# Kernel tuning notes

Measured on AMD Instinct MI355X. Metric: run time of the kernel, lower is better.

## Reference

```python
import jax, jax.numpy as jnp
import numpy as np

HIDDEN_DIM = 4096
NUM_EXPERTS = 64
TOP_K = 8
ROUTED_SCALING_FACTOR = 2.5
NUM_TOKENS = 16384


def setup_inputs() -> dict:
    key = jax.random.key(0)
    kx, kw = jax.random.split(key)
    x = jax.random.normal(kx, (NUM_TOKENS, HIDDEN_DIM), dtype=jnp.float32)
    # gate Linear weight (no bias): torch Linear stores [out, in]; we keep [in, out] for x @ W
    W = jax.random.normal(kw, (HIDDEN_DIM, NUM_EXPERTS), dtype=jnp.float32) * (1.0 / np.sqrt(HIDDEN_DIM))
    e_score_correction_bias = jnp.zeros((NUM_EXPERTS,), dtype=jnp.float32)
    return {"x": x, "W": W, "e_score_correction_bias": e_score_correction_bias}


def reference(x, W, e_score_correction_bias):
    # logits: [T, E]
    logits = jnp.einsum("td,de->te", x, W)
    scores = jax.nn.sigmoid(logits)
    scores_with_bias = scores + e_score_correction_bias
    # top-k over experts (sorted descending, matches torch.topk sorted=True)
    _, topk_indices = jax.lax.top_k(scores_with_bias, TOP_K)  # [T, k]
    # gather the UNBIASED scores at the selected experts
    topk_scores = jnp.take_along_axis(scores, topk_indices, axis=-1)  # [T, k]
    scores_sum = jnp.sum(topk_scores, axis=-1, keepdims=True) + 1e-20
    topk_weights = topk_scores / scores_sum * ROUTED_SCALING_FACTOR
    return topk_indices, topk_weights
```

## Files before the change

### kernel.cpp

```cpp
#include <hip/hip_runtime.h>
#include <math.h>

#define NT 16384
#define HD 4096
#define NE 64
#define TT 32
#define DC 64
#define NCH (HD / DC)
#define SXS 34
#define SLS 65
#define GAP_THRESH 4e-5f

__device__ __forceinline__ float fsig(float z) { return 1.0f / (1.0f + expf(-z)); }
__device__ __forceinline__ double dsig(double z) { return 1.0 / (1.0 + exp(-z)); }

__global__ __launch_bounds__(256) void moe_gate_f32(
    const float* __restrict__ X, const float* __restrict__ Wg,
    const float* __restrict__ bias, float* __restrict__ out,
    unsigned int* __restrict__ nflag, int* __restrict__ flags) {
  __shared__ float sX[DC][SXS];
  __shared__ float sW[DC][NE];
  __shared__ float sL[TT][SLS];
  __shared__ float sB[NE];

  const int tid   = threadIdx.x;
  const int tok0  = blockIdx.x * TT;
  const int tr    = tid >> 4;
  const int tc    = tid & 15;
  const int tok_s = tid >> 3;
  const int dv    = tid & 7;

  if (tid < NE) sB[tid] = bias[tid];

  float acc[2][4];
#pragma unroll
  for (int i = 0; i < 2; ++i)
#pragma unroll
    for (int j = 0; j < 4; ++j) acc[i][j] = 0.0f;

  const float* xrow = X + (size_t)(tok0 + tok_s) * HD + dv * 8;

  float4 xr[2], wr[4];
#pragma unroll
  for (int s = 0; s < 2; ++s) xr[s] = *(const float4*)(xrow + s * 4);
#pragma unroll
  for (int s = 0; s < 4; ++s)
    wr[s] = *(const float4*)(Wg + (size_t)(tid + 256 * s) * 4);

  for (int k = 0; k < NCH; ++k) {
    __syncthreads();
#pragma unroll
    for (int s = 0; s < 2; ++s) {
      const int d = dv * 8 + s * 4;
      sX[d + 0][tok_s] = xr[s].x;
      sX[d + 1][tok_s] = xr[s].y;
      sX[d + 2][tok_s] = xr[s].z;
      sX[d + 3][tok_s] = xr[s].w;
    }
#pragma unroll
    for (int s = 0; s < 4; ++s) {
      const int f = (tid + 256 * s) * 4;
      *(float4*)&sW[f >> 6][f & 63] = wr[s];
    }
    __syncthreads();
    if (k + 1 < NCH) {
      const float* xp = xrow + (k + 1) * DC;
      const float* wp = Wg + (size_t)(k + 1) * (DC * NE);
#pragma unroll
      for (int s = 0; s < 2; ++s) xr[s] = *(const float4*)(xp + s * 4);
#pragma unroll
      for (int s = 0; s < 4; ++s)
        wr[s] = *(const float4*)(wp + (size_t)(tid + 256 * s) * 4);
    }
#pragma unroll
    for (int dd = 0; dd < DC; ++dd) {
      const float2 xa = *(const float2*)&sX[dd][tr * 2];
      const float4 wa = *(const float4*)&sW[dd][tc * 4];
      acc[0][0] += xa.x * wa.x; acc[0][1] += xa.x * wa.y;
      acc[0][2] += xa.x * wa.z; acc[0][3] += xa.x * wa.w;
      acc[1][0] += xa.y * wa.x; acc[1][1] += xa.y * wa.y;
      acc[1][2] += xa.y * wa.z; acc[1][3] += xa.y * wa.w;
    }
  }

  __syncthreads();
#pragma unroll
  for (int i = 0; i < 2; ++i) {
    const int t = tr * 2 + i;
    sL[t][tc * 4 + 0] = fsig(acc[i][0]);
    sL[t][tc * 4 + 1] = fsig(acc[i][1]);
    sL[t][tc * 4 + 2] = fsig(acc[i][2]);
    sL[t][tc * 4 + 3] = fsig(acc[i][3]);
  }
  __syncthreads();

  if (tid < TT) {
    const int t = tid;
    float bsc[9]; int bix[9];
#pragma unroll
    for (int r = 0; r < 9; ++r) { bsc[r] = -INFINITY; bix[r] = 0; }
    for (int e = 0; e < NE; ++e) {
      float cb = sL[t][e] + sB[e];
      int   ci = e;
#pragma unroll
      for (int r = 0; r < 9; ++r) {
        const bool sw = cb > bsc[r];
        const float tb = bsc[r]; const int ti = bix[r];
        bsc[r] = sw ? cb : tb;  bix[r] = sw ? ci : ti;
        cb     = sw ? tb : cb;  ci     = sw ? ti : ci;
      }
    }
    float mg = bsc[0] - bsc[1];
#pragma unroll
    for (int r = 1; r < 8; ++r) mg = fminf(mg, bsc[r] - bsc[r + 1]);

    float us[8]; float sum = 1e-20f;
#pragma unroll
    for (int r = 0; r < 8; ++r) { us[r] = sL[t][bix[r]]; sum += us[r]; }
    const float sc = 2.5f / sum;
    const size_t o = (size_t)(tok0 + t) * 8;
    float4 i0 = {(float)bix[0], (float)bix[1], (float)bix[2], (float)bix[3]};
    float4 i1 = {(float)bix[4], (float)bix[5], (float)bix[6], (float)bix[7]};
    *(float4*)(out + o)     = i0;
    *(float4*)(out + o + 4) = i1;
    float* ow = out + (size_t)NT * 8;
    float4 w0 = {us[0] * sc, us[1] * sc, us[2] * sc, us[3] * sc};
    float4 w1 = {us[4] * sc, us[5] * sc, us[6] * sc, us[7] * sc};
    *(float4*)(ow + o)     = w0;
    *(float4*)(ow + o + 4) = w1;

    if (!(mg > GAP_THRESH)) {
      const unsigned int p = atomicAdd(nflag, 1u);
      if (p < NT) flags[p] = tok0 + t;
    }
  }
}

__global__ __launch_bounds__(256) void moe_gate_fix(
    const float* __restrict__ X, const float* __restrict__ Wg,
    const float* __restrict__ bias, float* __restrict__ out,
    const unsigned int* __restrict__ nflag, const int* __restrict__ flags) {
  __shared__ float  sx[HD];
  __shared__ double sP[NE][9];
  __shared__ double sS[NE];

  const int tid = threadIdx.x;
  unsigned int n = *nflag;
  if (n > NT) n = NT;

  for (unsigned int w = blockIdx.x; w < n; w += gridDim.x) {
    const int t = flags[w];
    __syncthreads();
    const float4* xv = (const float4*)(X + (size_t)t * HD);
#pragma unroll
    for (int i = 0; i < 4; ++i)
      ((float4*)sx)[tid + 256 * i] = xv[tid + 256 * i];
    __syncthreads();

    const int ep = (tid & 31) * 2;
    const int q  = tid >> 5;
    const float* wp = Wg + (size_t)(q * 512) * NE + ep;
    const float* xp = sx + q * 512;
    double a0 = 0.0, a1 = 0.0, b0 = 0.0, b1 = 0.0;
    for (int d = 0; d < 512; d += 2) {
      const double x0 = (double)xp[d];
      const double x1 = (double)xp[d + 1];
      const float2 w0 = *(const float2*)(wp + (size_t)d * NE);
      const float2 w1 = *(const float2*)(wp + (size_t)(d + 1) * NE);
      a0 += x0 * (double)w0.x; a1 += x0 * (double)w0.y;
      b0 += x1 * (double)w1.x; b1 += x1 * (double)w1.y;
    }
    sP[ep][q]     = a0 + b0;
    sP[ep + 1][q] = a1 + b1;
    __syncthreads();
    if (tid < NE) {
      double s = 0.0;
#pragma unroll
      for (int q8 = 0; q8 < 8; ++q8) s += sP[tid][q8];
      sS[tid] = dsig(s);
    }
    __syncthreads();
    if (tid == 0) {
      double bsc[8]; int bix[8];
#pragma unroll
      for (int r = 0; r < 8; ++r) { bsc[r] = -INFINITY; bix[r] = 0; }
      for (int e = 0; e < NE; ++e) {
        double cb = sS[e] + (double)bias[e];
        int   ci = e;
#pragma unroll
        for (int r = 0; r < 8; ++r) {
          const bool sw = cb > bsc[r];
          const double tb = bsc[r]; const int ti = bix[r];
          bsc[r] = sw ? cb : tb;  bix[r] = sw ? ci : ti;
          cb     = sw ? tb : cb;  ci     = sw ? ti : ci;
        }
      }
      double us[8]; double sum = 1e-20;
#pragma unroll
      for (int r = 0; r < 8; ++r) { us[r] = sS[bix[r]]; sum += us[r]; }
      const double sc = 2.5 / sum;
      const size_t o = (size_t)t * 8;
      float4 i0 = {(float)bix[0], (float)bix[1], (float)bix[2], (float)bix[3]};
      float4 i1 = {(float)bix[4], (float)bix[5], (float)bix[6], (float)bix[7]};
      *(float4*)(out + o)     = i0;
      *(float4*)(out + o + 4) = i1;
      float* ow = out + (size_t)NT * 8;
      float4 w0 = {(float)(us[0] * sc), (float)(us[1] * sc),
                   (float)(us[2] * sc), (float)(us[3] * sc)};
      float4 w1 = {(float)(us[4] * sc), (float)(us[5] * sc),
                   (float)(us[6] * sc), (float)(us[7] * sc)};
      *(float4*)(ow + o)     = w0;
      *(float4*)(ow + o + 4) = w1;
    }
  }
}

extern "C" void kernel_launch(void* const* d_in, const int* in_sizes, int n_in,
                              void* d_out, int out_size, void* d_ws, size_t ws_size,
                              hipStream_t stream) {
  const float* X  = (const float*)d_in[0];
  const float* Wg = (const float*)d_in[1];
  const float* b  = (const float*)d_in[2];
  float* out = (float*)d_out;
  unsigned int* nflag = (unsigned int*)d_ws;
  int* flags = (int*)((char*)d_ws + 64);
  hipMemsetAsync(d_ws, 0, 64, stream);
  hipLaunchKernelGGL(moe_gate_f32, dim3(NT / TT), dim3(256), 0, stream,
                     X, Wg, b, out, nflag, flags);
  hipLaunchKernelGGL(moe_gate_fix, dim3(256), dim3(256), 0, stream,
                     X, Wg, b, out, nflag, flags);
}
```

Baseline: 569.6 us.

## Split-K across waves with 8x8 register tiles and per-wave fix path

Measured after the change: 659.5 us. 15.8% more time.

```diff
diff --git a/kernel.cpp b/kernel.cpp
--- a/kernel.cpp
+++ b/kernel.cpp
@@ -4,95 +4,111 @@
 #define NT 16384
 #define HD 4096
 #define NE 64
-#define TT 32
-#define DC 64
-#define NCH (HD / DC)
-#define SXS 34
+#define TT 64
+#define KW 1024
+#define DC 32
+#define NCHW (KW / DC)
+#define SXS 68
 #define SLS 65
 #define GAP_THRESH 4e-5f
 
 __device__ __forceinline__ float fsig(float z) { return 1.0f / (1.0f + expf(-z)); }
 __device__ __forceinline__ double dsig(double z) { return 1.0 / (1.0 + exp(-z)); }
 
-__global__ __launch_bounds__(256) void moe_gate_f32(
+__global__ __launch_bounds__(256, 1) void moe_gate_f32(
     const float* __restrict__ X, const float* __restrict__ Wg,
     const float* __restrict__ bias, float* __restrict__ out,
     unsigned int* __restrict__ nflag, int* __restrict__ flags) {
-  __shared__ float sX[DC][SXS];
-  __shared__ float sW[DC][NE];
+  __shared__ float sX[4][2][DC][SXS];
+  __shared__ float sW[4][2][DC][NE];
   __shared__ float sL[TT][SLS];
   __shared__ float sB[NE];
 
-  const int tid   = threadIdx.x;
-  const int tok0  = blockIdx.x * TT;
-  const int tr    = tid >> 4;
-  const int tc    = tid & 15;
-  const int tok_s = tid >> 3;
-  const int dv    = tid & 7;
+  const int tid  = threadIdx.x;
+  const int wv   = tid >> 6;
+  const int ln   = tid & 63;
+  const int tok0 = blockIdx.x * TT;
+  const int tr8  = (ln & 7) * 8;
+  const int tc8  = (ln >> 3) * 8;
 
   if (tid < NE) sB[tid] = bias[tid];
 
-  float acc[2][4];
-#pragma unroll
-  for (int i = 0; i < 2; ++i)
-#pragma unroll
-    for (int j = 0; j < 4; ++j) acc[i][j] = 0.0f;
-
-  const float* xrow = X + (size_t)(tok0 + tok_s) * HD + dv * 8;
-
-  float4 xr[2], wr[4];
-#pragma unroll
-  for (int s = 0; s < 2; ++s) xr[s] = *(const float4*)(xrow + s * 4);
-#pragma unroll
-  for (int s = 0; s < 4; ++s)
-    wr[s] = *(const float4*)(Wg + (size_t)(tid + 256 * s) * 4);
-
-  for (int k = 0; k < NCH; ++k) {
+  float acc[8][8];
+#pragma unroll
+  for (int i = 0; i < 8; ++i)
+#pragma unroll
+    for (int j = 0; j < 8; ++j) acc[i][j] = 0.0f;
+
+  const float* xbase = X + (size_t)(tok0 + ln) * HD + wv * KW;
+  const float* wbase = Wg + (size_t)(wv * KW) * NE;
+
+  float4 xr[8], wr[8];
+#pragma unroll
+  for (int s = 0; s < 8; ++s) xr[s] = *(const float4*)(xbase + s * 4);
+#pragma unroll
+  for (int s = 0; s < 8; ++s) wr[s] = *(const float4*)(wbase + (ln + 64 * s) * 4);
+#pragma unroll
+  for (int s = 0; s < 8; ++s) {
+    const int d0 = s * 4;
+    sX[wv][0][d0 + 0][ln] = xr[s].x;
+    sX[wv][0][d0 + 1][ln] = xr[s].y;
+    sX[wv][0][d0 + 2][ln] = xr[s].z;
+    sX[wv][0][d0 + 3][ln] = xr[s].w;
+    *(float4*)&sW[wv][0][(ln >> 4) + 4 * s][(ln & 15) * 4] = wr[s];
+  }
+
+  for (int c = 0; c < NCHW; ++c) {
+    const int pb = c & 1;
+    if (c + 1 < NCHW) {
+      const float* xp = xbase + (c + 1) * DC;
+      const float* wp = wbase + (size_t)((c + 1) * DC) * NE;
+#pragma unroll
+      for (int s = 0; s < 8; ++s) xr[s] = *(const float4*)(xp + s * 4);
+#pragma unroll
+      for (int s = 0; s < 8; ++s) wr[s] = *(const float4*)(wp + (ln + 64 * s) * 4);
+    }
+#pragma unroll 8
+    for (int dd = 0; dd < DC; ++dd) {
+      const float4 xa = *(const float4*)&sX[wv][pb][dd][tr8];
+      const float4 xb = *(const float4*)&sX[wv][pb][dd][tr8 + 4];
+      const float4 wa = *(const float4*)&sW[wv][pb][dd][tc8];
+      const float4 wb = *(const float4*)&sW[wv][pb][dd][tc8 + 4];
+      const float xv[8] = {xa.x, xa.y, xa.z, xa.w, xb.x, xb.y, xb.z, xb.w};
+      const float wf[8] = {wa.x, wa.y, wa.z, wa.w, wb.x, wb.y, wb.z, wb.w};
+#pragma unroll
+      for (int i = 0; i < 8; ++i)
+#pragma unroll
+        for (int j = 0; j < 8; ++j) acc[i][j] += xv[i] * wf[j];
+    }
+    if (c + 1 < NCHW) {
+      const int nb = pb ^ 1;
+#pragma unroll
+      for (int s = 0; s < 8; ++s) {
+        const int d0 = s * 4;
+        sX[wv][nb][d0 + 0][ln] = xr[s].x;
+        sX[wv][nb][d0 + 1][ln] = xr[s].y;
+        sX[wv][nb][d0 + 2][ln] = xr[s].z;
+        sX[wv][nb][d0 + 3][ln] = xr[s].w;
+        *(float4*)&sW[wv][nb][(ln >> 4) + 4 * s][(ln & 15) * 4] = wr[s];
+      }
+    }
+  }
+
+  __syncthreads();
+  for (int w = 0; w < 4; ++w) {
+    if (wv == w) {
+#pragma unroll
+      for (int i = 0; i < 8; ++i)
+#pragma unroll
+        for (int jj = 0; jj < 8; ++jj) {
+          const int j = (jj + (ln & 7)) & 7;
+          float* p = &sL[tr8 + i][tc8 + j];
+          float v = (w == 0) ? acc[i][j] : (*p + acc[i][j]);
+          *p = (w == 3) ? fsig(v) : v;
+        }
+    }
     __syncthreads();
-#pragma unroll
-    for (int s = 0; s < 2; ++s) {
-      const int d = dv * 8 + s * 4;
-      sX[d + 0][tok_s] = xr[s].x;
-      sX[d + 1][tok_s] = xr[s].y;
-      sX[d + 2][tok_s] = xr[s].z;
-      sX[d + 3][tok_s] = xr[s].w;
-    }
-#pragma unroll
-    for (int s = 0; s < 4; ++s) {
-      const int f = (tid + 256 * s) * 4;
-      *(float4*)&sW[f >> 6][f & 63] = wr[s];
-    }
-    __syncthreads();
-    if (k + 1 < NCH) {
-      const float* xp = xrow + (k + 1) * DC;
-      const float* wp = Wg + (size_t)(k + 1) * (DC * NE);
-#pragma unroll
-      for (int s = 0; s < 2; ++s) xr[s] = *(const float4*)(xp + s * 4);
-#pragma unroll
-      for (int s = 0; s < 4; ++s)
-        wr[s] = *(const float4*)(wp + (size_t)(tid + 256 * s) * 4);
-    }
-#pragma unroll
-    for (int dd = 0; dd < DC; ++dd) {
-      const float2 xa = *(const float2*)&sX[dd][tr * 2];
-      const float4 wa = *(const float4*)&sW[dd][tc * 4];
-      acc[0][0] += xa.x * wa.x; acc[0][1] += xa.x * wa.y;
-      acc[0][2] += xa.x * wa.z; acc[0][3] += xa.x * wa.w;
-      acc[1][0] += xa.y * wa.x; acc[1][1] += xa.y * wa.y;
-      acc[1][2] += xa.y * wa.z; acc[1][3] += xa.y * wa.w;
-    }
-  }
-
-  __syncthreads();
-#pragma unroll
-  for (int i = 0; i < 2; ++i) {
-    const int t = tr * 2 + i;
-    sL[t][tc * 4 + 0] = fsig(acc[i][0]);
-    sL[t][tc * 4 + 1] = fsig(acc[i][1]);
-    sL[t][tc * 4 + 2] = fsig(acc[i][2]);
-    sL[t][tc * 4 + 3] = fsig(acc[i][3]);
-  }
-  __syncthreads();
+  }
 
   if (tid < TT) {
     const int t = tid;
@@ -136,56 +152,41 @@
   }
 }
 
-__global__ __launch_bounds__(256) void moe_gate_fix(
+__global__ __launch_bounds__(256, 1) void moe_gate_fix(
     const float* __restrict__ X, const float* __restrict__ Wg,
     const float* __restrict__ bias, float* __restrict__ out,
     const unsigned int* __restrict__ nflag, const int* __restrict__ flags) {
-  __shared__ float  sx[HD];
-  __shared__ double sP[NE][9];
-  __shared__ double sS[NE];
-
-  const int tid = threadIdx.x;
+  __shared__ double sS[4][NE];
+  const int tid = threadIdx.x, wv = tid >> 6, ln = tid & 63;
   unsigned int n = *nflag;
   if (n > NT) n = NT;
-
-  for (unsigned int w = blockIdx.x; w < n; w += gridDim.x) {
+  const unsigned int wid = blockIdx.x * 4 + wv;
+  const unsigned int wstride = gridDim.x * 4;
+
+  for (unsigned int w = wid; w < n; w += wstride) {
     const int t = flags[w];
-    __syncthreads();
-    const float4* xv = (const float4*)(X + (size_t)t * HD);
-#pragma unroll
-    for (int i = 0; i < 4; ++i)
-      ((float4*)sx)[tid + 256 * i] = xv[tid + 256 * i];
-    __syncthreads();
-
-    const int ep = (tid & 31) * 2;
-    const int q  = tid >> 5;
-    const float* wp = Wg + (size_t)(q * 512) * NE + ep;
-    const float* xp = sx + q * 512;
-    double a0 = 0.0, a1 = 0.0, b0 = 0.0, b1 = 0.0;
-    for (int d = 0; d < 512; d += 2) {
-      const double x0 = (double)xp[d];
-      const double x1 = (double)xp[d + 1];
-      const float2 w0 = *(const float2*)(wp + (size_t)d * NE);
-      const float2 w1 = *(const float2*)(wp + (size_t)(d + 1) * NE);
-      a0 += x0 * (double)w0.x; a1 += x0 * (double)w0.y;
-      b0 += x1 * (double)w1.x; b1 += x1 * (double)w1.y;
-    }
-    sP[ep][q]     = a0 + b0;
-    sP[ep + 1][q] = a1 + b1;
-    __syncthreads();
-    if (tid < NE) {
-      double s = 0.0;
-#pragma unroll
-      for (int q8 = 0; q8 < 8; ++q8) s += sP[tid][q8];
-      sS[tid] = dsig(s);
-    }
-    __syncthreads();
-    if (tid == 0) {
+    const float* xp = X + (size_t)t * HD;
+    const float* wp = Wg + ln;
+    double c0 = 0.0, c1 = 0.0, c2 = 0.0, c3 = 0.0;
+    for (int d = 0; d < HD; d += 4) {
+      const float4 x4 = *(const float4*)(xp + d);
+      const float w0 = wp[(size_t)(d + 0) * NE];
+      const float w1 = wp[(size_t)(d + 1) * NE];
+      const float w2 = wp[(size_t)(d + 2) * NE];
+      const float w3 = wp[(size_t)(d + 3) * NE];
+      c0 += (double)x4.x * (double)w0;
+      c1 += (double)x4.y * (double)w1;
+      c2 += (double)x4.z * (double)w2;
+      c3 += (double)x4.w * (double)w3;
+    }
+    sS[wv][ln] = dsig(((c0 + c1) + c2) + c3);
+
+    if (ln == 0) {
       double bsc[8]; int bix[8];
 #pragma unroll
       for (int r = 0; r < 8; ++r) { bsc[r] = -INFINITY; bix[r] = 0; }
       for (int e = 0; e < NE; ++e) {
-        double cb = sS[e] + (double)bias[e];
+        double cb = sS[wv][e] + (double)bias[e];
         int   ci = e;
 #pragma unroll
         for (int r = 0; r < 8; ++r) {
@@ -197,7 +198,7 @@
       }
       double us[8]; double sum = 1e-20;
 #pragma unroll
-      for (int r = 0; r < 8; ++r) { us[r] = sS[bix[r]]; sum += us[r]; }
+      for (int r = 0; r < 8; ++r) { us[r] = sS[wv][bix[r]]; sum += us[r]; }
       const double sc = 2.5 / sum;
       const size_t o = (size_t)t * 8;
       float4 i0 = {(float)bix[0], (float)bix[1], (float)bix[2], (float)bix[3]};
```

## Use split-bf16 MFMA for gate GEMM and batch the fp64 fix-up pass

Applied to the files above, without the earlier changes.

New measurement: 488.0 us. -14.3%, faster.

```diff
diff --git a/kernel.cpp b/kernel.cpp
--- a/kernel.cpp
+++ b/kernel.cpp
@@ -4,97 +4,149 @@
 #define NT 16384
 #define HD 4096
 #define NE 64
-#define TT 32
-#define DC 64
-#define NCH (HD / DC)
-#define SXS 34
-#define SLS 65
 #define GAP_THRESH 4e-5f
+
+typedef __bf16 bf16x8 __attribute__((ext_vector_type(8)));
+typedef float f32x4 __attribute__((ext_vector_type(4)));
+typedef unsigned int u32x4 __attribute__((ext_vector_type(4)));
+
+__device__ __attribute__((aligned(16))) unsigned short g_Wp[524288];
 
 __device__ __forceinline__ float fsig(float z) { return 1.0f / (1.0f + expf(-z)); }
 __device__ __forceinline__ double dsig(double z) { return 1.0 / (1.0 + exp(-z)); }
 
-__global__ __launch_bounds__(256) void moe_gate_f32(
-    const float* __restrict__ X, const float* __restrict__ Wg,
-    const float* __restrict__ bias, float* __restrict__ out,
-    unsigned int* __restrict__ nflag, int* __restrict__ flags) {
-  __shared__ float sX[DC][SXS];
-  __shared__ float sW[DC][NE];
-  __shared__ float sL[TT][SLS];
+__device__ __forceinline__ f32x4 mfma16(bf16x8 a, bf16x8 b, f32x4 c) {
+  return __builtin_amdgcn_mfma_f32_16x16x32_bf16(a, b, c, 0, 0, 0);
+}
+
+__device__ __forceinline__ unsigned bf16_rne(float f) {
+  const unsigned u = __builtin_bit_cast(unsigned, f);
+  return (u + 0x7FFFu + ((u >> 16) & 1u)) >> 16;
+}
+
+__device__ __forceinline__ void split2(float f0, float f1, unsigned& hi, unsigned& lo) {
+  const unsigned h0 = bf16_rne(f0), h1 = bf16_rne(f1);
+  const float hf0 = __builtin_bit_cast(float, h0 << 16);
+  const float hf1 = __builtin_bit_cast(float, h1 << 16);
+  const unsigned l0 = bf16_rne(f0 - hf0), l1 = bf16_rne(f1 - hf1);
+  hi = h0 | (h1 << 16);
+  lo = l0 | (l1 << 16);
+}
+
+__global__ __launch_bounds__(256) void prep_w(const float* __restrict__ Wg) {
+  const int g  = blockIdx.x * 256 + threadIdx.x;
+  const int l  = g & 63;
+  const int nf = (g >> 6) & 3;
+  const int kb = g >> 8;
+  const int d0 = kb * 32 + (l >> 4) * 8;
+  const int e  = nf * 16 + (l & 15);
+  u32x4 hi, lo;
+#pragma unroll
+  for (int p = 0; p < 4; ++p) {
+    const float f0 = Wg[(size_t)(d0 + 2 * p) * NE + e];
+    const float f1 = Wg[(size_t)(d0 + 2 * p + 1) * NE + e];
+    unsigned th, tl;
+    split2(f0, f1, th, tl);
+    hi[p] = th; lo[p] = tl;
+  }
+  *(u32x4*)(g_Wp + (size_t)g * 8) = hi;
+  *(u32x4*)(g_Wp + 262144 + (size_t)g * 8) = lo;
+}
+
+__global__ __launch_bounds__(256, 2) void moe_gate_f32(
+    const float* __restrict__ X, const float* __restrict__ bias,
+    float* __restrict__ out, unsigned int* __restrict__ nflag,
+    int* __restrict__ flags) {
+  __shared__ float sL[32][65];
   __shared__ float sB[NE];
 
-  const int tid   = threadIdx.x;
-  const int tok0  = blockIdx.x * TT;
-  const int tr    = tid >> 4;
-  const int tc    = tid & 15;
-  const int tok_s = tid >> 3;
-  const int dv    = tid & 7;
+  const int tid = threadIdx.x;
+  const int l   = tid & 63;
+  const int wv  = tid >> 6;
+  const int tg  = wv >> 1;
+  const int kh  = wv & 1;
+  const int tok0 = blockIdx.x * 32;
 
   if (tid < NE) sB[tid] = bias[tid];
 
-  float acc[2][4];
-#pragma unroll
-  for (int i = 0; i < 2; ++i)
-#pragma unroll
-    for (int j = 0; j < 4; ++j) acc[i][j] = 0.0f;
-
-  const float* xrow = X + (size_t)(tok0 + tok_s) * HD + dv * 8;
-
-  float4 xr[2], wr[4];
-#pragma unroll
-  for (int s = 0; s < 2; ++s) xr[s] = *(const float4*)(xrow + s * 4);
-#pragma unroll
-  for (int s = 0; s < 4; ++s)
-    wr[s] = *(const float4*)(Wg + (size_t)(tid + 256 * s) * 4);
-
-  for (int k = 0; k < NCH; ++k) {
-    __syncthreads();
-#pragma unroll
-    for (int s = 0; s < 2; ++s) {
-      const int d = dv * 8 + s * 4;
-      sX[d + 0][tok_s] = xr[s].x;
-      sX[d + 1][tok_s] = xr[s].y;
-      sX[d + 2][tok_s] = xr[s].z;
-      sX[d + 3][tok_s] = xr[s].w;
-    }
-#pragma unroll
-    for (int s = 0; s < 4; ++s) {
-      const int f = (tid + 256 * s) * 4;
-      *(float4*)&sW[f >> 6][f & 63] = wr[s];
-    }
-    __syncthreads();
-    if (k + 1 < NCH) {
-      const float* xp = xrow + (k + 1) * DC;
-      const float* wp = Wg + (size_t)(k + 1) * (DC * NE);
-#pragma unroll
-      for (int s = 0; s < 2; ++s) xr[s] = *(const float4*)(xp + s * 4);
-#pragma unroll
-      for (int s = 0; s < 4; ++s)
-        wr[s] = *(const float4*)(wp + (size_t)(tid + 256 * s) * 4);
-    }
-#pragma unroll
-    for (int dd = 0; dd < DC; ++dd) {
-      const float2 xa = *(const float2*)&sX[dd][tr * 2];
-      const float4 wa = *(const float4*)&sW[dd][tc * 4];
-      acc[0][0] += xa.x * wa.x; acc[0][1] += xa.x * wa.y;
-      acc[0][2] += xa.x * wa.z; acc[0][3] += xa.x * wa.w;
-      acc[1][0] += xa.y * wa.x; acc[1][1] += xa.y * wa.y;
-      acc[1][2] += xa.y * wa.z; acc[1][3] += xa.y * wa.w;
-    }
-  }
-
+  const float* xp = X + (size_t)(tok0 + tg * 16 + (l & 15)) * HD + kh * 2048 + (l >> 4) * 8;
+  const unsigned short* wp = g_Wp + kh * 131072 + l * 8;
+
+  f32x4 accm[4], accc[4];
+#pragma unroll
+  for (int nf = 0; nf < 4; ++nf) {
+    accm[nf] = f32x4{0.f, 0.f, 0.f, 0.f};
+    accc[nf] = f32x4{0.f, 0.f, 0.f, 0.f};
+  }
+
+  f32x4 a0c = __builtin_nontemporal_load((const f32x4*)xp);
+  f32x4 a1c = __builtin_nontemporal_load((const f32x4*)(xp + 4));
+  u32x4 bhc[4], blc[4], bhn[4], bln[4];
+#pragma unroll
+  for (int nf = 0; nf < 4; ++nf) {
+    bhc[nf] = *(const u32x4*)(wp + nf * 512);
+    blc[nf] = *(const u32x4*)(wp + 262144 + nf * 512);
+  }
+  f32x4 a0n, a1n;
+
+  for (int c = 0; c < 64; ++c) {
+    if (c < 63) {
+      const float* xn = xp + (c + 1) * 32;
+      a0n = __builtin_nontemporal_load((const f32x4*)xn);
+      a1n = __builtin_nontemporal_load((const f32x4*)(xn + 4));
+      const unsigned short* wn = wp + (size_t)(c + 1) * 2048;
+#pragma unroll
+      for (int nf = 0; nf < 4; ++nf) {
+        bhn[nf] = *(const u32x4*)(wn + nf * 512);
+        bln[nf] = *(const u32x4*)(wn + 262144 + nf * 512);
+      }
+    }
+    u32x4 ahu, alu;
+    {
+      unsigned th, tl;
+      split2(a0c[0], a0c[1], th, tl); ahu[0] = th; alu[0] = tl;
+      split2(a0c[2], a0c[3], th, tl); ahu[1] = th; alu[1] = tl;
+      split2(a1c[0], a1c[1], th, tl); ahu[2] = th; alu[2] = tl;
+      split2(a1c[2], a1c[3], th, tl); ahu[3] = th; alu[3] = tl;
+    }
+    const bf16x8 ah = __builtin_bit_cast(bf16x8, ahu);
+    const bf16x8 al = __builtin_bit_cast(bf16x8, alu);
+#pragma unroll
+    for (int nf = 0; nf < 4; ++nf) {
+      const bf16x8 bh = __builtin_bit_cast(bf16x8, bhc[nf]);
+      const bf16x8 bl = __builtin_bit_cast(bf16x8, blc[nf]);
+      accm[nf] = mfma16(ah, bh, accm[nf]);
+      accc[nf] = mfma16(ah, bl, accc[nf]);
+      accc[nf] = mfma16(al, bh, accc[nf]);
+      accc[nf] = mfma16(al, bl, accc[nf]);
+    }
+    if (c < 63) {
+      a0c = a0n; a1c = a1n;
+#pragma unroll
+      for (int nf = 0; nf < 4; ++nf) { bhc[nf] = bhn[nf]; blc[nf] = bln[nf]; }
+    }
+  }
+
+  if (kh == 0) {
+#pragma unroll
+    for (int nf = 0; nf < 4; ++nf)
+#pragma unroll
+      for (int r = 0; r < 4; ++r)
+        sL[tg * 16 + (l >> 4) * 4 + r][nf * 16 + (l & 15)] = accm[nf][r] + accc[nf][r];
+  }
   __syncthreads();
-#pragma unroll
-  for (int i = 0; i < 2; ++i) {
-    const int t = tr * 2 + i;
-    sL[t][tc * 4 + 0] = fsig(acc[i][0]);
-    sL[t][tc * 4 + 1] = fsig(acc[i][1]);
-    sL[t][tc * 4 + 2] = fsig(acc[i][2]);
-    sL[t][tc * 4 + 3] = fsig(acc[i][3]);
+  if (kh == 1) {
+#pragma unroll
+    for (int nf = 0; nf < 4; ++nf)
+#pragma unroll
+      for (int r = 0; r < 4; ++r) {
+        const int t = tg * 16 + (l >> 4) * 4 + r, e = nf * 16 + (l & 15);
+        sL[t][e] = fsig(sL[t][e] + (accm[nf][r] + accc[nf][r]));
+      }
   }
   __syncthreads();
 
-  if (tid < TT) {
+  if (tid < 32) {
     const int t = tid;
     float bsc[9]; int bix[9];
 #pragma unroll
@@ -136,57 +188,71 @@
   }
 }
 
-__global__ __launch_bounds__(256) void moe_gate_fix(
+#define FB 8
+__global__ __launch_bounds__(512) void moe_gate_fix(
     const float* __restrict__ X, const float* __restrict__ Wg,
     const float* __restrict__ bias, float* __restrict__ out,
     const unsigned int* __restrict__ nflag, const int* __restrict__ flags) {
-  __shared__ float  sx[HD];
-  __shared__ double sP[NE][9];
-  __shared__ double sS[NE];
+  __shared__ float  sx[FB][1024];
+  __shared__ double sP[8][FB][NE];
+  __shared__ double sS[FB][NE];
+  __shared__ int    stok[FB];
 
   const int tid = threadIdx.x;
+  const int e = tid & 63, q = tid >> 6;
   unsigned int n = *nflag;
   if (n > NT) n = NT;
 
-  for (unsigned int w = blockIdx.x; w < n; w += gridDim.x) {
-    const int t = flags[w];
+  for (unsigned int base = blockIdx.x * FB; base < n; base += gridDim.x * FB) {
+    const int cnt = (int)((n - base < (unsigned)FB) ? (n - base) : (unsigned)FB);
     __syncthreads();
-    const float4* xv = (const float4*)(X + (size_t)t * HD);
-#pragma unroll
-    for (int i = 0; i < 4; ++i)
-      ((float4*)sx)[tid + 256 * i] = xv[tid + 256 * i];
+    if (tid < FB) stok[tid] = flags[base + ((tid < cnt) ? tid : 0)];
+    double acc[FB];
+#pragma unroll
+    for (int t = 0; t < FB; ++t) acc[t] = 0.0;
+
+    for (int ch = 0; ch < 4; ++ch) {
+      __syncthreads();
+#pragma unroll
+      for (int s = 0; s < 4; ++s) {
+        const int idx = tid + 512 * s;
+        const int r = idx >> 8, c4 = (idx & 255) * 4;
+        *(float4*)&sx[r][c4] =
+            *(const float4*)(X + (size_t)stok[r] * HD + ch * 1024 + c4);
+      }
+      __syncthreads();
+      const int db = ch * 1024 + q * 128;
+#pragma unroll 4
+      for (int dd = 0; dd < 128; dd += 2) {
+        const double w0 = (double)Wg[(size_t)(db + dd) * NE + e];
+        const double w1 = (double)Wg[(size_t)(db + dd + 1) * NE + e];
+#pragma unroll
+        for (int t = 0; t < FB; ++t) {
+          const float2 xv = *(const float2*)&sx[t][q * 128 + dd];
+          acc[t] += (double)xv.x * w0;
+          acc[t] += (double)xv.y * w1;
+        }
+      }
+    }
+#pragma unroll
+    for (int t = 0; t < FB; ++t) sP[q][t][e] = acc[t];
     __syncthreads();
-
-    const int ep = (tid & 31) * 2;
-    const int q  = tid >> 5;
-    const float* wp = Wg + (size_t)(q * 512) * NE + ep;
-    const float* xp = sx + q * 512;
-    double a0 = 0.0, a1 = 0.0, b0 = 0.0, b1 = 0.0;
-    for (int d = 0; d < 512; d += 2) {
-      const double x0 = (double)xp[d];
-      const double x1 = (double)xp[d + 1];
-      const float2 w0 = *(const float2*)(wp + (size_t)d * NE);
-      const float2 w1 = *(const float2*)(wp + (size_t)(d + 1) * NE);
-      a0 += x0 * (double)w0.x; a1 += x0 * (double)w0.y;
-      b0 += x1 * (double)w1.x; b1 += x1 * (double)w1.y;
-    }
-    sP[ep][q]     = a0 + b0;
-    sP[ep + 1][q] = a1 + b1;
+    if (tid < FB * NE) {
+      const int t = tid >> 6;
+      double s = 0.0;
+#pragma unroll
+      for (int qq = 0; qq < 8; ++qq) s += sP[qq][t][e];
+      sS[t][e] = dsig(s);
+    }
     __syncthreads();
-    if (tid < NE) {
-      double s = 0.0;
-#pragma unroll
-      for (int q8 = 0; q8 < 8; ++q8) s += sP[tid][q8];
-      sS[tid] = dsig(s);
-    }
-    __syncthreads();
-    if (tid == 0) {
+    if (tid < cnt) {
+      const int t = tid;
       double bsc[8]; int bix[8];
 #pragma unroll
       for (int r = 0; r < 8; ++r) { bsc[r] = -INFINITY; bix[r] = 0; }
-      for (int e = 0; e < NE; ++e) {
-        double cb = sS[e] + (double)bias[e];
-        int   ci = e;
+      for (int ee = 0; ee < NE; ++ee) {
+        double cb = sS[t][ee] + (double)bias[ee];
+        int   ci = ee;
 #pragma unroll
         for (int r = 0; r < 8; ++r) {
           const bool sw = cb > bsc[r];
@@ -197,9 +263,9 @@
       }
       double us[8]; double sum = 1e-20;
 #pragma unroll
-      for (int r = 0; r < 8; ++r) { us[r] = sS[bix[r]]; sum += us[r]; }
+      for (int r = 0; r < 8; ++r) { us[r] = sS[t][bix[r]]; sum += us[r]; }
       const double sc = 2.5 / sum;
-      const size_t o = (size_t)t * 8;
+      const size_t o = (size_t)stok[t] * 8;
       float4 i0 = {(float)bix[0], (float)bix[1], (float)bix[2], (float)bix[3]};
       float4 i1 = {(float)bix[4], (float)bix[5], (float)bix[6], (float)bix[7]};
       *(float4*)(out + o)     = i0;
@@ -224,9 +290,10 @@
   float* out = (float*)d_out;
   unsigned int* nflag = (unsigned int*)d_ws;
   int* flags = (int*)((char*)d_ws + 64);
-  hipMemsetAsync(d_ws, 0, 64, stream);
-  hipLaunchKernelGGL(moe_gate_f32, dim3(NT / TT), dim3(256), 0, stream,
+  (void)hipMemsetAsync(d_ws, 0, 64, stream);
+  hipLaunchKernelGGL(prep_w, dim3(128), dim3(256), 0, stream, Wg);
+  hipLaunchKernelGGL(moe_gate_f32, dim3(NT / 32), dim3(256), 0, stream,
+                     X, b, out, nflag, flags);
+  hipLaunchKernelGGL(moe_gate_fix, dim3(256), dim3(512), 0, stream,
                      X, Wg, b, out, nflag, flags);
-  hipLaunchKernelGGL(moe_gate_fix, dim3(256), dim3(256), 0, stream,
-                     X, Wg, b, out, nflag, flags);
-}
+}
```
